# Kernel optimization log

Measured on AMD Instinct MI355X. Metric: run time of the kernel, lower is better.

Reference implementation:

```python
import jax, jax.numpy as jnp
import numpy as np

INF = 1e20


def setup_inputs() -> dict:
    key = jax.random.key(0)
    k1, k2, k3 = jax.random.split(key, 3)
    B, Q, M, F, D = 16, 64, 512, 16, 512
    return {
        "query_embed": jax.random.normal(k1, (B, Q, D), dtype=jnp.float32),
        "in_memory_embed": jax.random.normal(k2, (B, M, F, D), dtype=jnp.float32),
        "out_memory_embed": jax.random.normal(k3, (B, M, F, D), dtype=jnp.float32),
        "ctx_mask": jnp.ones((B, M, F), dtype=jnp.float32),
        "query_mask": jnp.ones((B, Q), dtype=jnp.float32),
    }


def reference(query_embed, in_memory_embed, out_memory_embed, ctx_mask, query_mask):
    # co-attention scores: [B, Q, M, F]
    attention = jnp.einsum("bqd,bmfd->bqmf", query_embed, in_memory_embed)
    # additive INF masking (torch: mask*att - (1-mask)*INF)
    cm = ctx_mask[:, None, :, :]            # [B,1,M,F]
    attention = cm * attention - (1.0 - cm) * INF
    qm = query_mask[:, :, None, None]       # [B,Q,1,1]
    attention = qm * attention - (1.0 - qm) * INF
    # NOTE: torch code computes a max-pool over Q for kb_feature_att but
    # immediately overwrites it with softmax of a ones/ctx mask -> dead code.
    mask = ctx_mask * 1.0 - (1.0 - ctx_mask) * INF        # [B,M,F]
    kb_feature_att = jax.nn.softmax(mask, axis=-1)        # [B,M,F]
    # weighted read over feature slots: [B,M,D]
    in_mem = jnp.einsum("bmf,bmfd->bmd", kb_feature_att, in_memory_embed)
    out_mem = out_memory_embed.sum(axis=2)                # [B,M,D]
    # max-pool over feature axis F -> [B,Q,M]
    att_qm = attention.max(axis=-1)
    probs = jax.nn.softmax(att_qm, axis=-1)               # over M
    new_query_embed = query_embed + jnp.einsum("bqm,bmd->bqd", probs, out_mem)
    probs2 = jax.nn.softmax(att_qm, axis=1)               # over Q
    in_mem = in_mem + jnp.einsum("bqm,bqd->bmd", probs2, new_query_embed)
    return (new_query_embed, in_mem, out_mem)
```

## Files before the change

kernel.cpp:

```cpp
#include <hip/hip_runtime.h>

#define INF_F 1e20f
#define B_ 16
#define Q_ 64
#define M_ 512
#define F_ 16
#define D_ 512

typedef __attribute__((ext_vector_type(8))) short short8v;
typedef __attribute__((ext_vector_type(4))) float f32x4;

static __device__ __forceinline__ float bits_f(unsigned u) { return __uint_as_float(u); }

static __device__ __forceinline__ void split4(float4 v, uint2& H, uint2& L) {
    unsigned hx = __float_as_uint(v.x) & 0xffff0000u, hy = __float_as_uint(v.y) & 0xffff0000u;
    unsigned hz = __float_as_uint(v.z) & 0xffff0000u, hw = __float_as_uint(v.w) & 0xffff0000u;
    H.x = (hx >> 16) | hy;
    H.y = (hz >> 16) | hw;
    L.x = (__float_as_uint(v.x - bits_f(hx)) >> 16) | (__float_as_uint(v.y - bits_f(hy)) & 0xffff0000u);
    L.y = (__float_as_uint(v.z - bits_f(hz)) >> 16) | (__float_as_uint(v.w - bits_f(hw)) & 0xffff0000u);
}

static __device__ __forceinline__ short8v mk8(uint2 a, uint2 b) {
    union { uint4 u; short8v s; } r;
    r.u = make_uint4(a.x, a.y, b.x, b.y);
    return r.s;
}

__global__ __launch_bounds__(256) void k_q_split(
    const float* __restrict__ q, short8v* __restrict__ qh, short8v* __restrict__ ql)
{
    int u = blockIdx.x * 256 + threadIdx.x;
    int row = u & 63, lg = (u >> 6) & 3, kc = (u >> 8) & 15, b = u >> 12;
    const float4* q4 = (const float4*)q;
    size_t s = (size_t)(b * 64 + row) * 128 + kc * 8 + lg * 2;
    float4 v0 = q4[s], v1 = q4[s + 1];
    uint2 H0, L0, H1, L1;
    split4(v0, H0, L0);
    split4(v1, H1, L1);
    uint4 H = make_uint4(H0.x, H0.y, H1.x, H1.y);
    uint4 L = make_uint4(L0.x, L0.y, L1.x, L1.y);
    *(uint4*)&qh[u] = H;
    *(uint4*)&ql[u] = L;
}

__global__ __launch_bounds__(256, 4) void k_att_mfma(
    const short8v* __restrict__ qhg, const short8v* __restrict__ qlg,
    const float* __restrict__ in_mem, const float* __restrict__ out_mem,
    const float* __restrict__ ctx_mask, const float* __restrict__ query_mask,
    float* __restrict__ att_qm, float* __restrict__ in_mem_base,
    float* __restrict__ out_mem_sum)
{
    const int bid = blockIdx.x;
    const int b    = bid & 15;
    const int role = (bid >> 4) & 1;
    const int m0   = (bid >> 5) * 8;
    const int t    = threadIdx.x;

    if (role == 0) {
        const int w = t >> 6, lane = t & 63;
        const int lr = lane & 15, lg = lane >> 4;
        const float4* in4 = (const float4*)in_mem;
        const size_t rb0 = (size_t)((b * M_ + m0 + 2 * w) * F_ + lr) * 128 + lg * 2;
        const size_t rb1 = rb0 + (size_t)F_ * 128;
        const int qb0 = b * 4096 + lg * 64 + lr;

        f32x4 acc[2][4];
        #pragma unroll
        for (int i = 0; i < 2; ++i)
            #pragma unroll
            for (int j = 0; j < 4; ++j) acc[i][j] = (f32x4){0, 0, 0, 0};

        float4 sc[4], sn[4];
        sc[0] = in4[rb0]; sc[1] = in4[rb0 + 1];
        sc[2] = in4[rb1]; sc[3] = in4[rb1 + 1];

#define MBODY(kc_, cur, nxt) do {                                              \
        if ((kc_) < 15) {                                                      \
            size_t o = (size_t)((kc_) + 1) * 8;                                \
            nxt[0] = in4[rb0 + o]; nxt[1] = in4[rb0 + o + 1];                  \
            nxt[2] = in4[rb1 + o]; nxt[3] = in4[rb1 + o + 1];                  \
        }                                                                      \
        uint2 H0, L0, H1, L1;                                                  \
        split4(cur[0], H0, L0); split4(cur[1], H1, L1);                        \
        short8v bh0 = mk8(H0, H1), bl0 = mk8(L0, L1);                          \
        split4(cur[2], H0, L0); split4(cur[3], H1, L1);                        \
        short8v bh1 = mk8(H0, H1), bl1 = mk8(L0, L1);                          \
        const int qb = qb0 + (kc_) * 256;                                      \
        _Pragma("unroll")                                                      \
        for (int tq = 0; tq < 4; ++tq) {                                       \
            short8v ah = qhg[qb + tq * 16];                                    \
            short8v al = qlg[qb + tq * 16];                                    \
            acc[0][tq] = __builtin_amdgcn_mfma_f32_16x16x32_bf16(ah, bh0, acc[0][tq], 0, 0, 0); \
            acc[0][tq] = __builtin_amdgcn_mfma_f32_16x16x32_bf16(ah, bl0, acc[0][tq], 0, 0, 0); \
            acc[0][tq] = __builtin_amdgcn_mfma_f32_16x16x32_bf16(al, bh0, acc[0][tq], 0, 0, 0); \
            acc[1][tq] = __builtin_amdgcn_mfma_f32_16x16x32_bf16(ah, bh1, acc[1][tq], 0, 0, 0); \
            acc[1][tq] = __builtin_amdgcn_mfma_f32_16x16x32_bf16(ah, bl1, acc[1][tq], 0, 0, 0); \
            acc[1][tq] = __builtin_amdgcn_mfma_f32_16x16x32_bf16(al, bh1, acc[1][tq], 0, 0, 0); \
        }                                                                      \
    } while (0)

        for (int it = 0; it < 8; ++it) {
            MBODY(2 * it, sc, sn);
            MBODY(2 * it + 1, sn, sc);
        }
#undef MBODY

        #pragma unroll
        for (int tm = 0; tm < 2; ++tm) {
            int m = m0 + 2 * w + tm;
            float cmv = ctx_mask[((size_t)b * M_ + m) * F_ + lr];
            #pragma unroll
            for (int tq = 0; tq < 4; ++tq) {
                #pragma unroll
                for (int rg = 0; rg < 4; ++rg) {
                    int q = tq * 16 + lg * 4 + rg;
                    float qmv = query_mask[b * Q_ + q];
                    float v = acc[tm][tq][rg];
                    v = cmv * v - (1.0f - cmv) * INF_F;
                    v = qmv * v - (1.0f - qmv) * INF_F;
                    #pragma unroll
                    for (int sh = 1; sh < 16; sh <<= 1) v = fmaxf(v, __shfl_xor(v, sh, 64));
                    if (lr == 0)
                        att_qm[((size_t)b * Q_ + q) * M_ + m] = v;
                }
            }
        }
    } else {
        const int th = t & 127;
        const bool is_in = (t < 128);
        const int msel = th >> 4, col4 = (th >> 1) & 7, half = th & 1;

        float wj[8];
        if (is_in) {
            const float* cm = ctx_mask + ((size_t)b * M_ + m0 + msel) * F_;
            float wv[16]; float mx = -INF_F;
            #pragma unroll
            for (int f = 0; f < 16; ++f) {
                float c = cm[f];
                float v = c - (1.0f - c) * INF_F;
                wv[f] = v; mx = fmaxf(mx, v);
            }
            float sum = 0.f;
            #pragma unroll
            for (int f = 0; f < 16; ++f) { wv[f] = __expf(wv[f] - mx); sum += wv[f]; }
            float inv = 1.0f / sum;
            #pragma unroll
            for (int j = 0; j < 8; ++j) wj[j] = wv[half * 8 + j] * inv;
        } else {
            #pragma unroll
            for (int j = 0; j < 8; ++j) wj[j] = 1.0f;
        }

        const float4* fsrc = is_in ? (const float4*)in_mem : (const float4*)out_mem;
        float4* fdst       = is_in ? (float4*)in_mem_base : (float4*)out_mem_sum;
        const size_t fbase = (size_t)((b * M_ + m0 + msel) * F_ + half * 8) * 128 + col4;
        const size_t fob   = (size_t)(b * M_ + m0 + msel) * 128 + col4;

        float4 fa[8], fb[8];
        #pragma unroll
        for (int j = 0; j < 8; ++j) fa[j] = fsrc[fbase + (size_t)j * 128];

#define FBODY(kc_, cur, nxt) do {                                              \
        if ((kc_) < 15) {                                                      \
            _Pragma("unroll")                                                  \
            for (int j = 0; j < 8; ++j)                                        \
                nxt[j] = fsrc[fbase + (size_t)j * 128 + ((kc_) + 1) * 8];      \
        }                                                                      \
        float4 s = make_float4(0, 0, 0, 0);                                    \
        _Pragma("unroll")                                                      \
        for (int j = 0; j < 8; ++j) {                                          \
            s.x += wj[j] * cur[j].x; s.y += wj[j] * cur[j].y;                  \
            s.z += wj[j] * cur[j].z; s.w += wj[j] * cur[j].w;                  \
        }                                                                      \
        s.x += __shfl_xor(s.x, 1, 64); s.y += __shfl_xor(s.y, 1, 64);          \
        s.z += __shfl_xor(s.z, 1, 64); s.w += __shfl_xor(s.w, 1, 64);          \
        if (half == 0) fdst[fob + (kc_) * 8] = s;                              \
    } while (0)

        for (int it = 0; it < 8; ++it) {
            FBODY(2 * it, fa, fb);
            FBODY(2 * it + 1, fb, fa);
        }
#undef FBODY
    }
}

__global__ __launch_bounds__(128) void k_new_query(
    const float* __restrict__ att, const float* __restrict__ query,
    const float* __restrict__ out_sum, float* __restrict__ new_q)
{
    __shared__ float P[8][512];
    int bid = blockIdx.x;
    int b = bid & 15, qc = bid >> 4;
    int t = threadIdx.x;
    {
        int qi = t >> 4, l16 = t & 15;
        const float* row = att + ((size_t)b * Q_ + qc * 8 + qi) * M_;
        float vals[32]; float mx = -INF_F;
        #pragma unroll
        for (int i = 0; i < 32; ++i) { vals[i] = row[l16 + i * 16]; mx = fmaxf(mx, vals[i]); }
        #pragma unroll
        for (int s = 1; s < 16; s <<= 1) mx = fmaxf(mx, __shfl_xor(mx, s, 64));
        float sm = 0.f;
        #pragma unroll
        for (int i = 0; i < 32; ++i) { vals[i] = __expf(vals[i] - mx); sm += vals[i]; }
        #pragma unroll
        for (int s = 1; s < 16; s <<= 1) sm += __shfl_xor(sm, s, 64);
        float inv = 1.0f / sm;
        #pragma unroll
        for (int i = 0; i < 32; ++i) P[qi][l16 + i * 16] = vals[i] * inv;
    }
    __syncthreads();
    int c = t;
    const float4* o4 = (const float4*)out_sum + (size_t)b * M_ * 128 + c;
    const float4* q4 = (const float4*)query + ((size_t)b * Q_ + qc * 8) * 128 + c;
    float4 acc[8];
    #pragma unroll
    for (int qi = 0; qi < 8; ++qi) acc[qi] = q4[(size_t)qi * 128];
    for (int mm = 0; mm < M_; mm += 4) {
        float4 o0 = o4[(size_t)(mm + 0) * 128];
        float4 o1 = o4[(size_t)(mm + 1) * 128];
        float4 o2 = o4[(size_t)(mm + 2) * 128];
        float4 o3 = o4[(size_t)(mm + 3) * 128];
        #pragma unroll
        for (int qi = 0; qi < 8; ++qi) {
            float4 p = *(const float4*)&P[qi][mm];
            acc[qi].x += p.x * o0.x + p.y * o1.x + p.z * o2.x + p.w * o3.x;
            acc[qi].y += p.x * o0.y + p.y * o1.y + p.z * o2.y + p.w * o3.y;
            acc[qi].z += p.x * o0.z + p.y * o1.z + p.z * o2.z + p.w * o3.z;
            acc[qi].w += p.x * o0.w + p.y * o1.w + p.z * o2.w + p.w * o3.w;
        }
    }
    float4* n4 = (float4*)new_q + ((size_t)b * Q_ + qc * 8) * 128 + c;
    #pragma unroll
    for (int qi = 0; qi < 8; ++qi) n4[(size_t)qi * 128] = acc[qi];
}

__global__ __launch_bounds__(128) void k_in_mem(
    const float* __restrict__ att, const float* __restrict__ new_q,
    float* __restrict__ in_mem_io)
{
    __shared__ float P[8][64];
    int bid = blockIdx.x;
    int b = bid & 15, mc = bid >> 4;
    int m0 = mc * 8;
    int t = threadIdx.x;
    {
        int mi = t >> 4, l16 = t & 15;
        float v[4]; float mx = -INF_F;
        #pragma unroll
        for (int i = 0; i < 4; ++i) {
            v[i] = att[((size_t)b * Q_ + l16 + i * 16) * M_ + m0 + mi];
            mx = fmaxf(mx, v[i]);
        }
        #pragma unroll
        for (int s = 1; s < 16; s <<= 1) mx = fmaxf(mx, __shfl_xor(mx, s, 64));
        float sm = 0.f;
        #pragma unroll
        for (int i = 0; i < 4; ++i) { v[i] = __expf(v[i] - mx); sm += v[i]; }
        #pragma unroll
        for (int s = 1; s < 16; s <<= 1) sm += __shfl_xor(sm, s, 64);
        float inv = 1.0f / sm;
        #pragma unroll
        for (int i = 0; i < 4; ++i) P[mi][l16 + i * 16] = v[i] * inv;
    }
    __syncthreads();
    int c = t;
    float4* io = (float4*)in_mem_io + ((size_t)b * M_ + m0) * 128 + c;
    const float4* n4 = (const float4*)new_q + (size_t)b * Q_ * 128 + c;
    float4 acc[8];
    #pragma unroll
    for (int mi = 0; mi < 8; ++mi) acc[mi] = io[(size_t)mi * 128];
    for (int q = 0; q < Q_; q += 4) {
        float4 n0 = n4[(size_t)(q + 0) * 128];
        float4 n1 = n4[(size_t)(q + 1) * 128];
        float4 n2 = n4[(size_t)(q + 2) * 128];
        float4 n3 = n4[(size_t)(q + 3) * 128];
        #pragma unroll
        for (int mi = 0; mi < 8; ++mi) {
            float4 p = *(const float4*)&P[mi][q];
            acc[mi].x += p.x * n0.x + p.y * n1.x + p.z * n2.x + p.w * n3.x;
            acc[mi].y += p.x * n0.y + p.y * n1.y + p.z * n2.y + p.w * n3.y;
            acc[mi].z += p.x * n0.z + p.y * n1.z + p.z * n2.z + p.w * n3.z;
            acc[mi].w += p.x * n0.w + p.y * n1.w + p.z * n2.w + p.w * n3.w;
        }
    }
    #pragma unroll
    for (int mi = 0; mi < 8; ++mi) io[(size_t)mi * 128] = acc[mi];
}

extern "C" void kernel_launch(void* const* d_in, const int* in_sizes, int n_in,
                              void* d_out, int out_size, void* d_ws, size_t ws_size,
                              hipStream_t stream)
{
    const float* query      = (const float*)d_in[0];
    const float* in_mem     = (const float*)d_in[1];
    const float* out_mem    = (const float*)d_in[2];
    const float* ctx_mask   = (const float*)d_in[3];
    const float* query_mask = (const float*)d_in[4];

    float* out = (float*)d_out;
    float* new_q      = out;
    float* in_mem_out = out + (size_t)B_*Q_*D_;
    float* out_mem_o  = in_mem_out + (size_t)B_*M_*D_;

    float* ws       = (float*)d_ws;
    float* att_qm   = ws;
    short8v* qh     = (short8v*)(ws + (size_t)B_*Q_*M_);
    short8v* ql     = qh + 65536;

    hipLaunchKernelGGL(k_q_split, dim3(256), dim3(256), 0, stream, query, qh, ql);
    hipLaunchKernelGGL(k_att_mfma, dim3((M_/8) * B_ * 2), dim3(256), 0, stream,
                       qh, ql, in_mem, out_mem, ctx_mask, query_mask,
                       att_qm, in_mem_out, out_mem_o);
    hipLaunchKernelGGL(k_new_query, dim3(8 * B_), dim3(128), 0, stream,
                       att_qm, query, out_mem_o, new_q);
    hipLaunchKernelGGL(k_in_mem, dim3(64 * B_), dim3(128), 0, stream,
                       att_qm, new_q, in_mem_out);
}
```

Measured before the change: 265.4 us.

## Split attention MFMA across query halves with LDS-staged Q and deeper prefetch

The attention kernel now launches three block roles per (batch, m-group): one does the feature-sum reductions and two each compute half of the queries. Query bf16 hi/lo fragments are staged in shared memory, and in_mem loads use a 4-deep register ring, with setprio around the MFMA groups. The new_query and in_mem kernels use half the rows per block, doubling their grid sizes for more parallelism. In exchange, in_mem is read twice by the attention blocks, shared memory rises to 64KB per block, and occupancy bounds drop to 2.

```diff
diff --git a/kernel.cpp b/kernel.cpp
--- a/kernel.cpp
+++ b/kernel.cpp
@@ -38,95 +38,28 @@
     uint2 H0, L0, H1, L1;
     split4(v0, H0, L0);
     split4(v1, H1, L1);
-    uint4 H = make_uint4(H0.x, H0.y, H1.x, H1.y);
-    uint4 L = make_uint4(L0.x, L0.y, L1.x, L1.y);
-    *(uint4*)&qh[u] = H;
-    *(uint4*)&ql[u] = L;
-}
-
-__global__ __launch_bounds__(256, 4) void k_att_mfma(
+    *(uint4*)&qh[u] = make_uint4(H0.x, H0.y, H1.x, H1.y);
+    *(uint4*)&ql[u] = make_uint4(L0.x, L0.y, L1.x, L1.y);
+}
+
+__global__ __launch_bounds__(256, 2) void k_att_mfma(
     const short8v* __restrict__ qhg, const short8v* __restrict__ qlg,
     const float* __restrict__ in_mem, const float* __restrict__ out_mem,
     const float* __restrict__ ctx_mask, const float* __restrict__ query_mask,
     float* __restrict__ att_qm, float* __restrict__ in_mem_base,
     float* __restrict__ out_mem_sum)
 {
+    __shared__ short8v QF[2][2048];
+
     const int bid = blockIdx.x;
-    const int b    = bid & 15;
-    const int role = (bid >> 4) & 1;
-    const int m0   = (bid >> 5) * 8;
-    const int t    = threadIdx.x;
-
-    if (role == 0) {
-        const int w = t >> 6, lane = t & 63;
-        const int lr = lane & 15, lg = lane >> 4;
-        const float4* in4 = (const float4*)in_mem;
-        const size_t rb0 = (size_t)((b * M_ + m0 + 2 * w) * F_ + lr) * 128 + lg * 2;
-        const size_t rb1 = rb0 + (size_t)F_ * 128;
-        const int qb0 = b * 4096 + lg * 64 + lr;
-
-        f32x4 acc[2][4];
-        #pragma unroll
-        for (int i = 0; i < 2; ++i)
-            #pragma unroll
-            for (int j = 0; j < 4; ++j) acc[i][j] = (f32x4){0, 0, 0, 0};
-
-        float4 sc[4], sn[4];
-        sc[0] = in4[rb0]; sc[1] = in4[rb0 + 1];
-        sc[2] = in4[rb1]; sc[3] = in4[rb1 + 1];
-
-#define MBODY(kc_, cur, nxt) do {                                              \
-        if ((kc_) < 15) {                                                      \
-            size_t o = (size_t)((kc_) + 1) * 8;                                \
-            nxt[0] = in4[rb0 + o]; nxt[1] = in4[rb0 + o + 1];                  \
-            nxt[2] = in4[rb1 + o]; nxt[3] = in4[rb1 + o + 1];                  \
-        }                                                                      \
-        uint2 H0, L0, H1, L1;                                                  \
-        split4(cur[0], H0, L0); split4(cur[1], H1, L1);                        \
-        short8v bh0 = mk8(H0, H1), bl0 = mk8(L0, L1);                          \
-        split4(cur[2], H0, L0); split4(cur[3], H1, L1);                        \
-        short8v bh1 = mk8(H0, H1), bl1 = mk8(L0, L1);                          \
-        const int qb = qb0 + (kc_) * 256;                                      \
-        _Pragma("unroll")                                                      \
-        for (int tq = 0; tq < 4; ++tq) {                                       \
-            short8v ah = qhg[qb + tq * 16];                                    \
-            short8v al = qlg[qb + tq * 16];                                    \
-            acc[0][tq] = __builtin_amdgcn_mfma_f32_16x16x32_bf16(ah, bh0, acc[0][tq], 0, 0, 0); \
-            acc[0][tq] = __builtin_amdgcn_mfma_f32_16x16x32_bf16(ah, bl0, acc[0][tq], 0, 0, 0); \
-            acc[0][tq] = __builtin_amdgcn_mfma_f32_16x16x32_bf16(al, bh0, acc[0][tq], 0, 0, 0); \
-            acc[1][tq] = __builtin_amdgcn_mfma_f32_16x16x32_bf16(ah, bh1, acc[1][tq], 0, 0, 0); \
-            acc[1][tq] = __builtin_amdgcn_mfma_f32_16x16x32_bf16(ah, bl1, acc[1][tq], 0, 0, 0); \
-            acc[1][tq] = __builtin_amdgcn_mfma_f32_16x16x32_bf16(al, bh1, acc[1][tq], 0, 0, 0); \
-        }                                                                      \
-    } while (0)
-
-        for (int it = 0; it < 8; ++it) {
-            MBODY(2 * it, sc, sn);
-            MBODY(2 * it + 1, sn, sc);
-        }
-#undef MBODY
-
-        #pragma unroll
-        for (int tm = 0; tm < 2; ++tm) {
-            int m = m0 + 2 * w + tm;
-            float cmv = ctx_mask[((size_t)b * M_ + m) * F_ + lr];
-            #pragma unroll
-            for (int tq = 0; tq < 4; ++tq) {
-                #pragma unroll
-                for (int rg = 0; rg < 4; ++rg) {
-                    int q = tq * 16 + lg * 4 + rg;
-                    float qmv = query_mask[b * Q_ + q];
-                    float v = acc[tm][tq][rg];
-                    v = cmv * v - (1.0f - cmv) * INF_F;
-                    v = qmv * v - (1.0f - qmv) * INF_F;
-                    #pragma unroll
-                    for (int sh = 1; sh < 16; sh <<= 1) v = fmaxf(v, __shfl_xor(v, sh, 64));
-                    if (lr == 0)
-                        att_qm[((size_t)b * Q_ + q) * M_ + m] = v;
-                }
-            }
-        }
-    } else {
+    const int b   = bid & 15;
+    const int t16 = bid >> 4;
+    const int r   = t16 % 3;
+    const int mg  = t16 / 3;
+    const int m0  = mg * 8;
+    const int t   = threadIdx.x;
+
+    if (r == 0) {
         const int th = t & 127;
         const bool is_in = (t < 128);
         const int msel = th >> 4, col4 = (th >> 1) & 7, half = th & 1;
@@ -178,11 +111,109 @@
         if (half == 0) fdst[fob + (kc_) * 8] = s;                              \
     } while (0)
 
+        #pragma unroll
         for (int it = 0; it < 8; ++it) {
             FBODY(2 * it, fa, fb);
             FBODY(2 * it + 1, fb, fa);
         }
 #undef FBODY
+        return;
+    }
+
+    const int qhalf = r - 1;
+    const int w = t >> 6, lane = t & 63;
+    const int lr = lane & 15, lg = lane >> 4;
+    const float4* in4 = (const float4*)in_mem;
+    const size_t rb0 = (size_t)((b * M_ + m0 + 2 * w) * F_ + lr) * 128 + lg * 2;
+    const size_t rb1 = rb0 + (size_t)F_ * 128;
+
+    float4 sb[4][4];
+    #pragma unroll
+    for (int s = 0; s < 4; ++s) {
+        size_t o = (size_t)s * 8;
+        sb[s][0] = in4[rb0 + o];     sb[s][1] = in4[rb0 + o + 1];
+        sb[s][2] = in4[rb1 + o];     sb[s][3] = in4[rb1 + o + 1];
+    }
+
+    #pragma unroll
+    for (int j = 0; j < 8; ++j) {
+        int i = t + j * 256;
+        int kc = i >> 7, lg2 = (i >> 5) & 3, row = i & 31;
+        int src = b * 4096 + kc * 256 + lg2 * 64 + qhalf * 32 + row;
+        QF[0][i] = qhg[src];
+        QF[1][i] = qlg[src];
+    }
+    __syncthreads();
+
+    f32x4 acc[2][2];
+    #pragma unroll
+    for (int i = 0; i < 2; ++i)
+        #pragma unroll
+        for (int j = 0; j < 2; ++j) acc[i][j] = (f32x4){0, 0, 0, 0};
+
+    short8v qA[4], qB[4];
+    qA[0] = QF[0][lg * 32 + lr];        qA[1] = QF[1][lg * 32 + lr];
+    qA[2] = QF[0][lg * 32 + 16 + lr];   qA[3] = QF[1][lg * 32 + 16 + lr];
+
+#define MBODY(kc_, QC, QN) do {                                                \
+        if ((kc_) + 1 < 16) {            \
+            int u = ((kc_) + 1) * 128 + lg * 32 + lr;                          \
+            QN[0] = QF[0][u];        QN[1] = QF[1][u];                         \
+            QN[2] = QF[0][u + 16];   QN[3] = QF[1][u + 16];                    \
+        }                                                                      \
+        {                                                                      \
+            const int sl = (kc_) & 3;                                          \
+            uint2 H0, L0, H1, L1;                                              \
+            split4(sb[sl][0], H0, L0); split4(sb[sl][1], H1, L1);              \
+            short8v bh0 = mk8(H0, H1), bl0 = mk8(L0, L1);                      \
+            split4(sb[sl][2], H0, L0); split4(sb[sl][3], H1, L1);              \
+            short8v bh1 = mk8(H0, H1), bl1 = mk8(L0, L1);                      \
+            if ((kc_) + 4 < 16) {       \
+                size_t o = (size_t)((kc_) + 4) * 8;                            \
+                sb[sl][0] = in4[rb0 + o];  sb[sl][1] = in4[rb0 + o + 1];       \
+                sb[sl][2] = in4[rb1 + o];  sb[sl][3] = in4[rb1 + o + 1];       \
+            }                                                                  \
+            __builtin_amdgcn_s_setprio(1);                                     \
+            _Pragma("unroll")                                                  \
+            for (int tq = 0; tq < 2; ++tq) {                                   \
+                short8v ah = QC[2 * tq], al = QC[2 * tq + 1];                  \
+                acc[0][tq] = __builtin_amdgcn_mfma_f32_16x16x32_bf16(ah, bh0, acc[0][tq], 0, 0, 0); \
+                acc[0][tq] = __builtin_amdgcn_mfma_f32_16x16x32_bf16(ah, bl0, acc[0][tq], 0, 0, 0); \
+                acc[0][tq] = __builtin_amdgcn_mfma_f32_16x16x32_bf16(al, bh0, acc[0][tq], 0, 0, 0); \
+                acc[1][tq] = __builtin_amdgcn_mfma_f32_16x16x32_bf16(ah, bh1, acc[1][tq], 0, 0, 0); \
+                acc[1][tq] = __builtin_amdgcn_mfma_f32_16x16x32_bf16(ah, bl1, acc[1][tq], 0, 0, 0); \
+                acc[1][tq] = __builtin_amdgcn_mfma_f32_16x16x32_bf16(al, bh1, acc[1][tq], 0, 0, 0); \
+            }                                                                  \
+            __builtin_amdgcn_s_setprio(0);                                     \
+        }                                                                      \
+    } while (0)
+
+    #pragma unroll
+    for (int it = 0; it < 8; ++it) {
+        MBODY(2 * it,     qA, qB);
+        MBODY(2 * it + 1, qB, qA);
+    }
+#undef MBODY
+
+    #pragma unroll
+    for (int tm = 0; tm < 2; ++tm) {
+        int m = m0 + 2 * w + tm;
+        float cmv = ctx_mask[((size_t)b * M_ + m) * F_ + lr];
+        #pragma unroll
+        for (int tq = 0; tq < 2; ++tq) {
+            #pragma unroll
+            for (int rg = 0; rg < 4; ++rg) {
+                int q = qhalf * 32 + tq * 16 + lg * 4 + rg;
+                float qmv = query_mask[b * Q_ + q];
+                float v = acc[tm][tq][rg];
+                v = cmv * v - (1.0f - cmv) * INF_F;
+                v = qmv * v - (1.0f - qmv) * INF_F;
+                #pragma unroll
+                for (int sh = 1; sh < 16; sh <<= 1) v = fmaxf(v, __shfl_xor(v, sh, 64));
+                if (lr == 0)
+                    att_qm[((size_t)b * Q_ + q) * M_ + m] = v;
+            }
+        }
     }
 }
 
@@ -190,41 +221,41 @@
     const float* __restrict__ att, const float* __restrict__ query,
     const float* __restrict__ out_sum, float* __restrict__ new_q)
 {
-    __shared__ float P[8][512];
+    __shared__ float P[4][512];
     int bid = blockIdx.x;
     int b = bid & 15, qc = bid >> 4;
     int t = threadIdx.x;
     {
-        int qi = t >> 4, l16 = t & 15;
-        const float* row = att + ((size_t)b * Q_ + qc * 8 + qi) * M_;
-        float vals[32]; float mx = -INF_F;
-        #pragma unroll
-        for (int i = 0; i < 32; ++i) { vals[i] = row[l16 + i * 16]; mx = fmaxf(mx, vals[i]); }
-        #pragma unroll
-        for (int s = 1; s < 16; s <<= 1) mx = fmaxf(mx, __shfl_xor(mx, s, 64));
+        int qi = t >> 5, l32 = t & 31;
+        const float* row = att + ((size_t)b * Q_ + qc * 4 + qi) * M_;
+        float vals[16]; float mx = -INF_F;
+        #pragma unroll
+        for (int i = 0; i < 16; ++i) { vals[i] = row[l32 + i * 32]; mx = fmaxf(mx, vals[i]); }
+        #pragma unroll
+        for (int s = 1; s < 32; s <<= 1) mx = fmaxf(mx, __shfl_xor(mx, s, 32));
         float sm = 0.f;
         #pragma unroll
-        for (int i = 0; i < 32; ++i) { vals[i] = __expf(vals[i] - mx); sm += vals[i]; }
-        #pragma unroll
-        for (int s = 1; s < 16; s <<= 1) sm += __shfl_xor(sm, s, 64);
+        for (int i = 0; i < 16; ++i) { vals[i] = __expf(vals[i] - mx); sm += vals[i]; }
+        #pragma unroll
+        for (int s = 1; s < 32; s <<= 1) sm += __shfl_xor(sm, s, 32);
         float inv = 1.0f / sm;
         #pragma unroll
-        for (int i = 0; i < 32; ++i) P[qi][l16 + i * 16] = vals[i] * inv;
+        for (int i = 0; i < 16; ++i) P[qi][l32 + i * 32] = vals[i] * inv;
     }
     __syncthreads();
     int c = t;
     const float4* o4 = (const float4*)out_sum + (size_t)b * M_ * 128 + c;
-    const float4* q4 = (const float4*)query + ((size_t)b * Q_ + qc * 8) * 128 + c;
-    float4 acc[8];
-    #pragma unroll
-    for (int qi = 0; qi < 8; ++qi) acc[qi] = q4[(size_t)qi * 128];
+    const float4* q4 = (const float4*)query + ((size_t)b * Q_ + qc * 4) * 128 + c;
+    float4 acc[4];
+    #pragma unroll
+    for (int qi = 0; qi < 4; ++qi) acc[qi] = q4[(size_t)qi * 128];
     for (int mm = 0; mm < M_; mm += 4) {
         float4 o0 = o4[(size_t)(mm + 0) * 128];
         float4 o1 = o4[(size_t)(mm + 1) * 128];
         float4 o2 = o4[(size_t)(mm + 2) * 128];
         float4 o3 = o4[(size_t)(mm + 3) * 128];
         #pragma unroll
-        for (int qi = 0; qi < 8; ++qi) {
+        for (int qi = 0; qi < 4; ++qi) {
             float4 p = *(const float4*)&P[qi][mm];
             acc[qi].x += p.x * o0.x + p.y * o1.x + p.z * o2.x + p.w * o3.x;
             acc[qi].y += p.x * o0.y + p.y * o1.y + p.z * o2.y + p.w * o3.y;
@@ -232,53 +263,53 @@
             acc[qi].w += p.x * o0.w + p.y * o1.w + p.z * o2.w + p.w * o3.w;
         }
     }
-    float4* n4 = (float4*)new_q + ((size_t)b * Q_ + qc * 8) * 128 + c;
-    #pragma unroll
-    for (int qi = 0; qi < 8; ++qi) n4[(size_t)qi * 128] = acc[qi];
+    float4* n4 = (float4*)new_q + ((size_t)b * Q_ + qc * 4) * 128 + c;
+    #pragma unroll
+    for (int qi = 0; qi < 4; ++qi) n4[(size_t)qi * 128] = acc[qi];
 }
 
 __global__ __launch_bounds__(128) void k_in_mem(
     const float* __restrict__ att, const float* __restrict__ new_q,
     float* __restrict__ in_mem_io)
 {
-    __shared__ float P[8][64];
+    __shared__ float P[4][64];
     int bid = blockIdx.x;
     int b = bid & 15, mc = bid >> 4;
-    int m0 = mc * 8;
+    int m0 = mc * 4;
     int t = threadIdx.x;
     {
-        int mi = t >> 4, l16 = t & 15;
-        float v[4]; float mx = -INF_F;
-        #pragma unroll
-        for (int i = 0; i < 4; ++i) {
-            v[i] = att[((size_t)b * Q_ + l16 + i * 16) * M_ + m0 + mi];
+        int mi = t >> 5, l32 = t & 31;
+        float v[2]; float mx = -INF_F;
+        #pragma unroll
+        for (int i = 0; i < 2; ++i) {
+            v[i] = att[((size_t)b * Q_ + l32 + i * 32) * M_ + m0 + mi];
             mx = fmaxf(mx, v[i]);
         }
         #pragma unroll
-        for (int s = 1; s < 16; s <<= 1) mx = fmaxf(mx, __shfl_xor(mx, s, 64));
+        for (int s = 1; s < 32; s <<= 1) mx = fmaxf(mx, __shfl_xor(mx, s, 32));
         float sm = 0.f;
         #pragma unroll
-        for (int i = 0; i < 4; ++i) { v[i] = __expf(v[i] - mx); sm += v[i]; }
-        #pragma unroll
-        for (int s = 1; s < 16; s <<= 1) sm += __shfl_xor(sm, s, 64);
+        for (int i = 0; i < 2; ++i) { v[i] = __expf(v[i] - mx); sm += v[i]; }
+        #pragma unroll
+        for (int s = 1; s < 32; s <<= 1) sm += __shfl_xor(sm, s, 32);
         float inv = 1.0f / sm;
         #pragma unroll
-        for (int i = 0; i < 4; ++i) P[mi][l16 + i * 16] = v[i] * inv;
+        for (int i = 0; i < 2; ++i) P[mi][l32 + i * 32] = v[i] * inv;
     }
     __syncthreads();
     int c = t;
     float4* io = (float4*)in_mem_io + ((size_t)b * M_ + m0) * 128 + c;
     const float4* n4 = (const float4*)new_q + (size_t)b * Q_ * 128 + c;
-    float4 acc[8];
-    #pragma unroll
-    for (int mi = 0; mi < 8; ++mi) acc[mi] = io[(size_t)mi * 128];
+    float4 acc[4];
+    #pragma unroll
+    for (int mi = 0; mi < 4; ++mi) acc[mi] = io[(size_t)mi * 128];
     for (int q = 0; q < Q_; q += 4) {
         float4 n0 = n4[(size_t)(q + 0) * 128];
         float4 n1 = n4[(size_t)(q + 1) * 128];
         float4 n2 = n4[(size_t)(q + 2) * 128];
         float4 n3 = n4[(size_t)(q + 3) * 128];
         #pragma unroll
-        for (int mi = 0; mi < 8; ++mi) {
+        for (int mi = 0; mi < 4; ++mi) {
             float4 p = *(const float4*)&P[mi][q];
             acc[mi].x += p.x * n0.x + p.y * n1.x + p.z * n2.x + p.w * n3.x;
             acc[mi].y += p.x * n0.y + p.y * n1.y + p.z * n2.y + p.w * n3.y;
@@ -287,7 +318,7 @@
         }
     }
     #pragma unroll
-    for (int mi = 0; mi < 8; ++mi) io[(size_t)mi * 128] = acc[mi];
+    for (int mi = 0; mi < 4; ++mi) io[(size_t)mi * 128] = acc[mi];
 }
 
 extern "C" void kernel_launch(void* const* d_in, const int* in_sizes, int n_in,
@@ -311,11 +342,11 @@
     short8v* ql     = qh + 65536;
 
     hipLaunchKernelGGL(k_q_split, dim3(256), dim3(256), 0, stream, query, qh, ql);
-    hipLaunchKernelGGL(k_att_mfma, dim3((M_/8) * B_ * 2), dim3(256), 0, stream,
+    hipLaunchKernelGGL(k_att_mfma, dim3(64 * 3 * B_), dim3(256), 0, stream,
                        qh, ql, in_mem, out_mem, ctx_mask, query_mask,
                        att_qm, in_mem_out, out_mem_o);
-    hipLaunchKernelGGL(k_new_query, dim3(8 * B_), dim3(128), 0, stream,
+    hipLaunchKernelGGL(k_new_query, dim3(16 * B_), dim3(128), 0, stream,
                        att_qm, query, out_mem_o, new_q);
-    hipLaunchKernelGGL(k_in_mem, dim3(64 * B_), dim3(128), 0, stream,
+    hipLaunchKernelGGL(k_in_mem, dim3(128 * B_), dim3(128), 0, stream,
                        att_qm, new_q, in_mem_out);
 }
```

New measurement: 281.4 us. +6.0%, slower.

## Stage query splits in LDS and rebalance fused MFMA and reduction blocks

Applied to the files above, without the earlier changes.

The attention kernel now uses 512-thread blocks, each covering 32 memory rows instead of 8. The query hi/lo bf16 splits are staged through shared memory in four chunks and reused by all 8 waves, instead of every wave reading them from global memory. The reduction role is rebalanced so two of every three blocks do the feature-slot reduction, with in/out streams interleaved across adjacent lanes. The MFMA section is also given raised wave priority. The cost is more barriers per block and a coarser grid (768 blocks), which may lower occupancy or leave load imbalance between the two roles.

```diff
diff --git a/kernel.cpp b/kernel.cpp
--- a/kernel.cpp
+++ b/kernel.cpp
@@ -38,128 +38,153 @@
     uint2 H0, L0, H1, L1;
     split4(v0, H0, L0);
     split4(v1, H1, L1);
-    uint4 H = make_uint4(H0.x, H0.y, H1.x, H1.y);
-    uint4 L = make_uint4(L0.x, L0.y, L1.x, L1.y);
-    *(uint4*)&qh[u] = H;
-    *(uint4*)&ql[u] = L;
-}
-
-__global__ __launch_bounds__(256, 4) void k_att_mfma(
+    *(uint4*)&qh[u] = make_uint4(H0.x, H0.y, H1.x, H1.y);
+    *(uint4*)&ql[u] = make_uint4(L0.x, L0.y, L1.x, L1.y);
+}
+
+__global__ __launch_bounds__(512, 3) void k_fused(
     const short8v* __restrict__ qhg, const short8v* __restrict__ qlg,
     const float* __restrict__ in_mem, const float* __restrict__ out_mem,
     const float* __restrict__ ctx_mask, const float* __restrict__ query_mask,
     float* __restrict__ att_qm, float* __restrict__ in_mem_base,
     float* __restrict__ out_mem_sum)
 {
+    __shared__ short8v QH[1024];
+    __shared__ short8v QL[1024];
+
     const int bid = blockIdx.x;
-    const int b    = bid & 15;
-    const int role = (bid >> 4) & 1;
-    const int m0   = (bid >> 5) * 8;
-    const int t    = threadIdx.x;
-
-    if (role == 0) {
-        const int w = t >> 6, lane = t & 63;
-        const int lr = lane & 15, lg = lane >> 4;
+    const int t   = threadIdx.x;
+
+    if (bid % 3 == 0) {
+        const int k  = bid / 3;
+        const int b  = k >> 4;
+        const int m0 = (k & 15) * 32;
+        const int w  = t >> 6;
+        const int lane = t & 63;
+        const int lr = lane & 15;
+        const int lg = lane >> 4;
         const float4* in4 = (const float4*)in_mem;
-        const size_t rb0 = (size_t)((b * M_ + m0 + 2 * w) * F_ + lr) * 128 + lg * 2;
-        const size_t rb1 = rb0 + (size_t)F_ * 128;
-        const int qb0 = b * 4096 + lg * 64 + lr;
-
-        f32x4 acc[2][4];
-        #pragma unroll
-        for (int i = 0; i < 2; ++i)
+        const int qgb = b * 4096;
+
+        #pragma unroll
+        for (int p = 0; p < 2; ++p) {
+            f32x4 acc[2][4];
             #pragma unroll
-            for (int j = 0; j < 4; ++j) acc[i][j] = (f32x4){0, 0, 0, 0};
-
-        float4 sc[4], sn[4];
-        sc[0] = in4[rb0]; sc[1] = in4[rb0 + 1];
-        sc[2] = in4[rb1]; sc[3] = in4[rb1 + 1];
-
-#define MBODY(kc_, cur, nxt) do {                                              \
-        if ((kc_) < 15) {                                                      \
-            size_t o = (size_t)((kc_) + 1) * 8;                                \
-            nxt[0] = in4[rb0 + o]; nxt[1] = in4[rb0 + o + 1];                  \
-            nxt[2] = in4[rb1 + o]; nxt[3] = in4[rb1 + o + 1];                  \
-        }                                                                      \
-        uint2 H0, L0, H1, L1;                                                  \
-        split4(cur[0], H0, L0); split4(cur[1], H1, L1);                        \
-        short8v bh0 = mk8(H0, H1), bl0 = mk8(L0, L1);                          \
-        split4(cur[2], H0, L0); split4(cur[3], H1, L1);                        \
-        short8v bh1 = mk8(H0, H1), bl1 = mk8(L0, L1);                          \
-        const int qb = qb0 + (kc_) * 256;                                      \
-        _Pragma("unroll")                                                      \
-        for (int tq = 0; tq < 4; ++tq) {                                       \
-            short8v ah = qhg[qb + tq * 16];                                    \
-            short8v al = qlg[qb + tq * 16];                                    \
-            acc[0][tq] = __builtin_amdgcn_mfma_f32_16x16x32_bf16(ah, bh0, acc[0][tq], 0, 0, 0); \
-            acc[0][tq] = __builtin_amdgcn_mfma_f32_16x16x32_bf16(ah, bl0, acc[0][tq], 0, 0, 0); \
-            acc[0][tq] = __builtin_amdgcn_mfma_f32_16x16x32_bf16(al, bh0, acc[0][tq], 0, 0, 0); \
-            acc[1][tq] = __builtin_amdgcn_mfma_f32_16x16x32_bf16(ah, bh1, acc[1][tq], 0, 0, 0); \
-            acc[1][tq] = __builtin_amdgcn_mfma_f32_16x16x32_bf16(ah, bl1, acc[1][tq], 0, 0, 0); \
-            acc[1][tq] = __builtin_amdgcn_mfma_f32_16x16x32_bf16(al, bh1, acc[1][tq], 0, 0, 0); \
-        }                                                                      \
-    } while (0)
-
-        for (int it = 0; it < 8; ++it) {
-            MBODY(2 * it, sc, sn);
-            MBODY(2 * it + 1, sn, sc);
-        }
-#undef MBODY
-
-        #pragma unroll
-        for (int tm = 0; tm < 2; ++tm) {
-            int m = m0 + 2 * w + tm;
-            float cmv = ctx_mask[((size_t)b * M_ + m) * F_ + lr];
+            for (int i = 0; i < 2; ++i)
+                #pragma unroll
+                for (int j = 0; j < 4; ++j) acc[i][j] = (f32x4){0, 0, 0, 0};
+
+            const size_t rb0 = ((size_t)((b * M_ + m0 + w * 4 + 2 * p) * F_) + lr) * 128 + lg * 2;
+            const size_t rb1 = rb0 + (size_t)F_ * 128;
+            float4 s0[4], s1[4];
+
             #pragma unroll
-            for (int tq = 0; tq < 4; ++tq) {
+            for (int qp = 0; qp < 4; ++qp) {
+                __syncthreads();
+                {
+                    const size_t o = (size_t)(qp * 4) * 8;
+                    s0[0] = in4[rb0 + o]; s0[1] = in4[rb0 + o + 1];
+                    s0[2] = in4[rb1 + o]; s0[3] = in4[rb1 + o + 1];
+                }
+                QH[t]       = qhg[qgb + qp * 1024 + t];
+                QH[t + 512] = qhg[qgb + qp * 1024 + t + 512];
+                QL[t]       = qlg[qgb + qp * 1024 + t];
+                QL[t + 512] = qlg[qgb + qp * 1024 + t + 512];
+                __syncthreads();
+
                 #pragma unroll
-                for (int rg = 0; rg < 4; ++rg) {
-                    int q = tq * 16 + lg * 4 + rg;
-                    float qmv = query_mask[b * Q_ + q];
-                    float v = acc[tm][tq][rg];
-                    v = cmv * v - (1.0f - cmv) * INF_F;
-                    v = qmv * v - (1.0f - qmv) * INF_F;
+                for (int kq = 0; kq < 4; ++kq) {
+                    float4* sc = (kq & 1) ? s1 : s0;
+                    float4* sn = (kq & 1) ? s0 : s1;
+                    if (kq < 3) {
+                        const size_t o = (size_t)(qp * 4 + kq + 1) * 8;
+                        sn[0] = in4[rb0 + o]; sn[1] = in4[rb0 + o + 1];
+                        sn[2] = in4[rb1 + o]; sn[3] = in4[rb1 + o + 1];
+                    }
+                    uint2 H0, L0, H1, L1;
+                    split4(sc[0], H0, L0); split4(sc[1], H1, L1);
+                    short8v bh0 = mk8(H0, H1), bl0 = mk8(L0, L1);
+                    split4(sc[2], H0, L0); split4(sc[3], H1, L1);
+                    short8v bh1 = mk8(H0, H1), bl1 = mk8(L0, L1);
+                    const int qu = kq * 256 + lg * 64 + lr;
+                    __builtin_amdgcn_s_setprio(1);
                     #pragma unroll
-                    for (int sh = 1; sh < 16; sh <<= 1) v = fmaxf(v, __shfl_xor(v, sh, 64));
-                    if (lr == 0)
-                        att_qm[((size_t)b * Q_ + q) * M_ + m] = v;
+                    for (int tq = 0; tq < 4; ++tq) {
+                        short8v ah = QH[qu + tq * 16];
+                        short8v al = QL[qu + tq * 16];
+                        acc[0][tq] = __builtin_amdgcn_mfma_f32_16x16x32_bf16(ah, bh0, acc[0][tq], 0, 0, 0);
+                        acc[0][tq] = __builtin_amdgcn_mfma_f32_16x16x32_bf16(ah, bl0, acc[0][tq], 0, 0, 0);
+                        acc[0][tq] = __builtin_amdgcn_mfma_f32_16x16x32_bf16(al, bh0, acc[0][tq], 0, 0, 0);
+                        acc[1][tq] = __builtin_amdgcn_mfma_f32_16x16x32_bf16(ah, bh1, acc[1][tq], 0, 0, 0);
+                        acc[1][tq] = __builtin_amdgcn_mfma_f32_16x16x32_bf16(ah, bl1, acc[1][tq], 0, 0, 0);
+                        acc[1][tq] = __builtin_amdgcn_mfma_f32_16x16x32_bf16(al, bh1, acc[1][tq], 0, 0, 0);
+                    }
+                    __builtin_amdgcn_s_setprio(0);
                 }
             }
-        }
+
+            #pragma unroll
+            for (int tm = 0; tm < 2; ++tm) {
+                int m = m0 + w * 4 + 2 * p + tm;
+                float cmv = ctx_mask[((size_t)b * M_ + m) * F_ + lr];
+                #pragma unroll
+                for (int tq = 0; tq < 4; ++tq) {
+                    #pragma unroll
+                    for (int rg = 0; rg < 4; ++rg) {
+                        int q = tq * 16 + lg * 4 + rg;
+                        float qmv = query_mask[b * Q_ + q];
+                        float v = acc[tm][tq][rg];
+                        v = cmv * v - (1.0f - cmv) * INF_F;
+                        v = qmv * v - (1.0f - qmv) * INF_F;
+                        #pragma unroll
+                        for (int sh = 1; sh < 16; sh <<= 1) v = fmaxf(v, __shfl_xor(v, sh, 64));
+                        if (lr == 0)
+                            att_qm[((size_t)b * Q_ + q) * M_ + m] = v;
+                    }
+                }
+            }
+        }
+        return;
+    }
+
+    const int s    = bid - bid / 3 - 1;
+    const int b    = s >> 5;
+    const int m0   = (s & 31) * 16;
+    const int msel = t >> 5;
+    const int r5   = t & 31;
+    const int c    = r5 >> 2;
+    const int half = (r5 >> 1) & 1;
+    const int strm = r5 & 1;
+
+    float wj[8];
+    if (strm == 0) {
+        const float* cm = ctx_mask + ((size_t)b * M_ + m0 + msel) * F_;
+        float wv[16]; float mx = -INF_F;
+        #pragma unroll
+        for (int f = 0; f < 16; ++f) {
+            float cv = cm[f];
+            float v = cv - (1.0f - cv) * INF_F;
+            wv[f] = v; mx = fmaxf(mx, v);
+        }
+        float sum = 0.f;
+        #pragma unroll
+        for (int f = 0; f < 16; ++f) { wv[f] = __expf(wv[f] - mx); sum += wv[f]; }
+        float inv = 1.0f / sum;
+        #pragma unroll
+        for (int j = 0; j < 8; ++j) wj[j] = wv[half * 8 + j] * inv;
     } else {
-        const int th = t & 127;
-        const bool is_in = (t < 128);
-        const int msel = th >> 4, col4 = (th >> 1) & 7, half = th & 1;
-
-        float wj[8];
-        if (is_in) {
-            const float* cm = ctx_mask + ((size_t)b * M_ + m0 + msel) * F_;
-            float wv[16]; float mx = -INF_F;
-            #pragma unroll
-            for (int f = 0; f < 16; ++f) {
-                float c = cm[f];
-                float v = c - (1.0f - c) * INF_F;
-                wv[f] = v; mx = fmaxf(mx, v);
-            }
-            float sum = 0.f;
-            #pragma unroll
-            for (int f = 0; f < 16; ++f) { wv[f] = __expf(wv[f] - mx); sum += wv[f]; }
-            float inv = 1.0f / sum;
-            #pragma unroll
-            for (int j = 0; j < 8; ++j) wj[j] = wv[half * 8 + j] * inv;
-        } else {
-            #pragma unroll
-            for (int j = 0; j < 8; ++j) wj[j] = 1.0f;
-        }
-
-        const float4* fsrc = is_in ? (const float4*)in_mem : (const float4*)out_mem;
-        float4* fdst       = is_in ? (float4*)in_mem_base : (float4*)out_mem_sum;
-        const size_t fbase = (size_t)((b * M_ + m0 + msel) * F_ + half * 8) * 128 + col4;
-        const size_t fob   = (size_t)(b * M_ + m0 + msel) * 128 + col4;
-
-        float4 fa[8], fb[8];
-        #pragma unroll
-        for (int j = 0; j < 8; ++j) fa[j] = fsrc[fbase + (size_t)j * 128];
+        #pragma unroll
+        for (int j = 0; j < 8; ++j) wj[j] = 1.0f;
+    }
+
+    const float4* fsrc = strm ? (const float4*)out_mem : (const float4*)in_mem;
+    float4* fdst       = strm ? (float4*)out_mem_sum : (float4*)in_mem_base;
+    const size_t fbase = ((size_t)((b * M_ + m0 + msel) * F_ + half * 8)) * 128 + c;
+    const size_t obase = (size_t)(b * M_ + m0 + msel) * 128 + c;
+
+    float4 fa[8], fb[8];
+    #pragma unroll
+    for (int j = 0; j < 8; ++j) fa[j] = fsrc[fbase + (size_t)j * 128];
 
 #define FBODY(kc_, cur, nxt) do {                                              \
         if ((kc_) < 15) {                                                      \
@@ -167,23 +192,23 @@
             for (int j = 0; j < 8; ++j)                                        \
                 nxt[j] = fsrc[fbase + (size_t)j * 128 + ((kc_) + 1) * 8];      \
         }                                                                      \
-        float4 s = make_float4(0, 0, 0, 0);                                    \
+        float4 s4 = make_float4(0, 0, 0, 0);                                   \
         _Pragma("unroll")                                                      \
         for (int j = 0; j < 8; ++j) {                                          \
-            s.x += wj[j] * cur[j].x; s.y += wj[j] * cur[j].y;                  \
-            s.z += wj[j] * cur[j].z; s.w += wj[j] * cur[j].w;                  \
+            s4.x += wj[j] * cur[j].x; s4.y += wj[j] * cur[j].y;                \
+            s4.z += wj[j] * cur[j].z; s4.w += wj[j] * cur[j].w;                \
         }                                                                      \
-        s.x += __shfl_xor(s.x, 1, 64); s.y += __shfl_xor(s.y, 1, 64);          \
-        s.z += __shfl_xor(s.z, 1, 64); s.w += __shfl_xor(s.w, 1, 64);          \
-        if (half == 0) fdst[fob + (kc_) * 8] = s;                              \
+        s4.x += __shfl_xor(s4.x, 2, 64); s4.y += __shfl_xor(s4.y, 2, 64);      \
+        s4.z += __shfl_xor(s4.z, 2, 64); s4.w += __shfl_xor(s4.w, 2, 64);      \
+        if (half == 0) fdst[obase + (kc_) * 8] = s4;                           \
     } while (0)
 
-        for (int it = 0; it < 8; ++it) {
-            FBODY(2 * it, fa, fb);
-            FBODY(2 * it + 1, fb, fa);
-        }
+    #pragma unroll
+    for (int it = 0; it < 8; ++it) {
+        FBODY(2 * it, fa, fb);
+        FBODY(2 * it + 1, fb, fa);
+    }
 #undef FBODY
-    }
 }
 
 __global__ __launch_bounds__(128) void k_new_query(
@@ -311,7 +336,7 @@
     short8v* ql     = qh + 65536;
 
     hipLaunchKernelGGL(k_q_split, dim3(256), dim3(256), 0, stream, query, qh, ql);
-    hipLaunchKernelGGL(k_att_mfma, dim3((M_/8) * B_ * 2), dim3(256), 0, stream,
+    hipLaunchKernelGGL(k_fused, dim3(768), dim3(512), 0, stream,
                        qh, ql, in_mem, out_mem, ctx_mask, query_mask,
                        att_qm, in_mem_out, out_mem_o);
     hipLaunchKernelGGL(k_new_query, dim3(8 * B_), dim3(128), 0, stream,
```

Result: slower. 283.6 us (+6.8%).
